# Performance work log

Measured on AMD Instinct MI355X. Metric: run time of the kernel, lower is better.

Reference implementation:

```python
import jax, jax.numpy as jnp
import numpy as np

EMBED_DIM = 1024
NUM_HEADS = 16
BLOCK_SIZE = 128
GLOBAL_EVERY = 24


def make_block_sparse_mask(seq_len):
    # 0 where allowed, -inf where disallowed. Allowed iff same block, or
    # either position lies in a 'global' block (block index % global_every == 0).
    bi = jnp.arange(seq_len) // BLOCK_SIZE
    is_global = (bi % GLOBAL_EVERY) == 0
    allowed = (bi[:, None] == bi[None, :]) | is_global[:, None] | is_global[None, :]
    return jnp.where(allowed, 0.0, -jnp.inf).astype(jnp.float32)


def setup_inputs() -> dict:
    key = jax.random.key(0)
    k_x, k_w, k_wo = jax.random.split(key, 3)
    B, L, D = 1, 4096, EMBED_DIM
    x = jax.random.normal(k_x, (B, L, D), dtype=jnp.float32)
    # nn.MultiheadAttention params: packed in_proj [3D, D] + bias [3D], out_proj [D, D] + bias [D]
    w_qkv = jax.random.normal(k_w, (3 * D, D), dtype=jnp.float32) * 0.02
    b_qkv = jnp.zeros((3 * D,), dtype=jnp.float32)
    w_out = jax.random.normal(k_wo, (D, D), dtype=jnp.float32) * 0.02
    b_out = jnp.zeros((D,), dtype=jnp.float32)
    return {"x": x, "w_qkv": w_qkv, "b_qkv": b_qkv, "w_out": w_out, "b_out": b_out}


def reference(x, w_qkv, b_qkv, w_out, b_out):
    B, L, D = x.shape
    H = NUM_HEADS
    hd = D // H
    mask = make_block_sparse_mask(L)  # [L, L] additive
    qkv = x @ w_qkv.T + b_qkv  # [B, L, 3D]
    q, k, v = jnp.split(qkv, 3, axis=-1)
    # [B, H, L, hd]
    q = q.reshape(B, L, H, hd).transpose(0, 2, 1, 3)
    k = k.reshape(B, L, H, hd).transpose(0, 2, 1, 3)
    v = v.reshape(B, L, H, hd).transpose(0, 2, 1, 3)
    scale = 1.0 / jnp.sqrt(jnp.asarray(hd, dtype=x.dtype))
    scores = jnp.einsum('bhqd,bhkd->bhqk', q * scale, k) + mask  # [B, H, L, L]
    attn = jax.nn.softmax(scores, axis=-1)
    out = jnp.einsum('bhqk,bhkd->bhqd', attn, v)  # [B, H, L, hd]
    out = out.transpose(0, 2, 1, 3).reshape(B, L, D)
    return out @ w_out.T + b_out
```

## Files before the change

### kernel.cpp

```cpp
#include <hip/hip_runtime.h>
#include <hip/hip_bf16.h>
#include <math.h>


#define SEQ 4096
#define DIM 1024
#define NHEADS 16
#define HDIM 64
#define BS 128
#define ESTRIDE 136

using short8 = __attribute__((ext_vector_type(8))) short;
using floatx4 = __attribute__((ext_vector_type(4))) float;

__device__ __forceinline__ float bf2f(short s) {
  unsigned u = ((unsigned)(unsigned short)s) << 16;
  return __uint_as_float(u);
}

__device__ __forceinline__ unsigned pack_bf16(float a, float b) {
  __hip_bfloat16 ba = __float2bfloat16(a);
  __hip_bfloat16 bb = __float2bfloat16(b);
  return ((unsigned)*(unsigned short*)&bb << 16) | (unsigned)*(unsigned short*)&ba;
}

__device__ __forceinline__ void gld_lds16(const __hip_bfloat16* g, __hip_bfloat16* l) {
  __builtin_amdgcn_global_load_lds(
      (const __attribute__((address_space(1))) unsigned int*)g,
      (__attribute__((address_space(3))) unsigned int*)l, 16, 0, 0);
}

__global__ __launch_bounds__(256) void downcast3(
    const float* __restrict__ x, const float* __restrict__ wq,
    const float* __restrict__ wo, __hip_bfloat16* __restrict__ xd,
    __hip_bfloat16* __restrict__ wqd, __hip_bfloat16* __restrict__ wod) {
  int id = blockIdx.x;
  const float* src;
  __hip_bfloat16* dst;
  int base;
  if (id < 4096) { src = x; dst = xd; base = id; }
  else if (id < 7168) { src = wq; dst = wqd; base = id - 4096; }
  else { src = wo; dst = wod; base = id - 7168; }
  int i = (base * 256 + threadIdx.x) * 4;
  float4 v = *(const float4*)(src + i);
  __hip_bfloat16 b0 = __float2bfloat16(v.x);
  __hip_bfloat16 b1 = __float2bfloat16(v.y);
  __hip_bfloat16 b2 = __float2bfloat16(v.z);
  __hip_bfloat16 b3 = __float2bfloat16(v.w);
  ushort4 packed = {*(unsigned short*)&b0, *(unsigned short*)&b1,
                    *(unsigned short*)&b2, *(unsigned short*)&b3};
  *(ushort4*)(((unsigned short*)dst) + i) = packed;
}

__global__ __launch_bounds__(256) void gemm_qkv(const __hip_bfloat16* __restrict__ Amat,
                                                const __hip_bfloat16* __restrict__ Wmat,
                                                const float* __restrict__ Bias,
                                                __hip_bfloat16* __restrict__ qkv) {
  __shared__ __align__(16) char pool[128 * ESTRIDE * 2];
  __hip_bfloat16* Asmem = (__hip_bfloat16*)pool;
  __hip_bfloat16* Bsmem = (__hip_bfloat16*)(pool + 8192);
  __hip_bfloat16* Ep = (__hip_bfloat16*)pool;

  const int Kd = DIM;
  const int t = threadIdx.x;
  const int w = t >> 6;
  const int lane = t & 63;
  const int fr = lane & 15;
  const int quad = lane >> 4;
  const int wm = w >> 1, wn = w & 1;

  int id = blockIdx.x;
  int xcd = id & 7, j = id >> 3;
  int m_idx = xcd + (j & 3) * 8;
  int n_idx = j >> 2;
  const int m0 = m_idx * 128;
  const int n0 = n_idx * 128;
  const int s = n0 >> 10;
  const int cc0 = n0 & 1023;
  const bool vmode = (s == 2);

  const __hip_bfloat16* APtr = vmode ? Amat + (size_t)m0 * Kd : Wmat + (size_t)n0 * Kd;
  const __hip_bfloat16* BPtr = vmode ? Wmat + (size_t)n0 * Kd : Amat + (size_t)m0 * Kd;

  floatx4 acc[4][4];
#pragma unroll
  for (int i = 0; i < 4; ++i)
#pragma unroll
    for (int jj = 0; jj < 4; ++jj) acc[i][jj] = (floatx4){0.f, 0.f, 0.f, 0.f};

  for (int kk = 0; kk < Kd / 32; ++kk) {
#pragma unroll
    for (int jj = 0; jj < 2; ++jj) {
      int c = jj * 256 + t;
      int ldso = (jj * 256 + w * 64) * 8;
      gld_lds16(APtr + (size_t)(c >> 2) * Kd + kk * 32 + (c & 3) * 8, &Asmem[ldso]);
      gld_lds16(BPtr + (size_t)(c >> 2) * Kd + kk * 32 + (c & 3) * 8, &Bsmem[ldso]);
    }
    __syncthreads();
    short8 af[4], bf_[4];
#pragma unroll
    for (int mt = 0; mt < 4; ++mt)
      af[mt] = *(const short8*)&Asmem[(wm * 64 + mt * 16 + fr) * 32 + quad * 8];
#pragma unroll
    for (int nt = 0; nt < 4; ++nt)
      bf_[nt] = *(const short8*)&Bsmem[(wn * 64 + nt * 16 + fr) * 32 + quad * 8];
#pragma unroll
    for (int mt = 0; mt < 4; ++mt)
#pragma unroll
      for (int nt = 0; nt < 4; ++nt)
        acc[mt][nt] = __builtin_amdgcn_mfma_f32_16x16x32_bf16(af[mt], bf_[nt],
                                                              acc[mt][nt], 0, 0, 0);
    __syncthreads();
  }

#pragma unroll
  for (int nt = 0; nt < 4; ++nt) {
    int dcol = wn * 64 + nt * 16 + fr;
#pragma unroll
    for (int mt = 0; mt < 4; ++mt) {
      int drow0 = wm * 64 + mt * 16 + quad * 4;
      ushort4 pk;
      unsigned short* pks = (unsigned short*)&pk;
#pragma unroll
      for (int i = 0; i < 4; ++i) {
        __hip_bfloat16 bb = __float2bfloat16(acc[mt][nt][i]);
        pks[i] = *(unsigned short*)&bb;
      }
      *(ushort4*)&Ep[dcol * ESTRIDE + drow0] = pk;
    }
  }
  __syncthreads();

  if (!vmode) {
    __hip_bfloat16* dst = qkv + (size_t)s * SEQ * DIM;
#pragma unroll
    for (int rr = 0; rr < 8; ++rr) {
      int m = rr * 16 + (t >> 4);
      int ch = (t & 15) * 8;
      short8 v8 = *(const short8*)&Ep[m * ESTRIDE + ch];
      float4 b0 = *(const float4*)&Bias[n0 + ch];
      float4 b1 = *(const float4*)&Bias[n0 + ch + 4];
      float bb[8] = {b0.x, b0.y, b0.z, b0.w, b1.x, b1.y, b1.z, b1.w};
      short8 o8;
#pragma unroll
      for (int k = 0; k < 8; ++k) {
        __hip_bfloat16 ob = __float2bfloat16(bf2f(v8[k]) + bb[k]);
        o8[k] = *(short*)&ob;
      }
      *(short8*)&dst[(size_t)(m0 + m) * DIM + cc0 + ch] = o8;
    }
  } else {
    __hip_bfloat16* vt = qkv + 2ull * SEQ * DIM;
#pragma unroll
    for (int rr = 0; rr < 8; ++rr) {
      int nrow = rr * 16 + (t >> 4);
      int ch = (t & 15) * 8;
      float bv = Bias[n0 + nrow];
      short8 v8 = *(const short8*)&Ep[nrow * ESTRIDE + ch];
      short8 o8;
#pragma unroll
      for (int k = 0; k < 8; ++k) {
        __hip_bfloat16 ob = __float2bfloat16(bf2f(v8[k]) + bv);
        o8[k] = *(short*)&ob;
      }
      *(short8*)&vt[(size_t)(cc0 + nrow) * SEQ + m0 + ch] = o8;
    }
  }
}

__global__ __launch_bounds__(256) void gemm_out(const __hip_bfloat16* __restrict__ Amat,
                                                const __hip_bfloat16* __restrict__ Wmat,
                                                const float* __restrict__ Bias,
                                                float* __restrict__ out) {
  __shared__ __align__(16) __hip_bfloat16 Asmem[128 * 32];
  __shared__ __align__(16) __hip_bfloat16 Bsmem[64 * 32];
  const int Kd = DIM;
  const int t = threadIdx.x;
  const int w = t >> 6;
  const int lane = t & 63;
  const int fr = lane & 15;
  const int quad = lane >> 4;
  const int wm = w >> 1, wn = w & 1;
  int id = blockIdx.x;
  int xcd = id & 7, j = id >> 3;
  int m_idx = xcd + (j & 3) * 8;
  int n_idx = j >> 2;
  const int m0 = m_idx * 128;
  const int n0 = n_idx * 64;
  const __hip_bfloat16* Ablk = Amat + (size_t)m0 * Kd;
  const __hip_bfloat16* Bblk = Wmat + (size_t)n0 * Kd;
  floatx4 acc[4][2];
#pragma unroll
  for (int i = 0; i < 4; ++i)
#pragma unroll
    for (int jj = 0; jj < 2; ++jj) acc[i][jj] = (floatx4){0.f, 0.f, 0.f, 0.f};
  for (int kk = 0; kk < Kd / 32; ++kk) {
#pragma unroll
    for (int jj = 0; jj < 2; ++jj) {
      int c = jj * 256 + t;
      int ldso = (jj * 256 + w * 64) * 8;
      gld_lds16(Ablk + (size_t)(c >> 2) * Kd + kk * 32 + (c & 3) * 8, &Asmem[ldso]);
    }
    gld_lds16(Bblk + (size_t)(t >> 2) * Kd + kk * 32 + (t & 3) * 8, &Bsmem[t * 8]);
    __syncthreads();
    short8 af[4], bf_[2];
#pragma unroll
    for (int mt = 0; mt < 4; ++mt)
      af[mt] = *(const short8*)&Asmem[(wm * 64 + mt * 16 + fr) * 32 + quad * 8];
#pragma unroll
    for (int nt = 0; nt < 2; ++nt)
      bf_[nt] = *(const short8*)&Bsmem[(wn * 32 + nt * 16 + fr) * 32 + quad * 8];
#pragma unroll
    for (int mt = 0; mt < 4; ++mt)
#pragma unroll
      for (int nt = 0; nt < 2; ++nt)
        acc[mt][nt] = __builtin_amdgcn_mfma_f32_16x16x32_bf16(af[mt], bf_[nt],
                                                              acc[mt][nt], 0, 0, 0);
    __syncthreads();
  }
#pragma unroll
  for (int nt = 0; nt < 2; ++nt) {
    int n = n0 + wn * 32 + nt * 16 + fr;
    float bv = Bias[n];
#pragma unroll
    for (int mt = 0; mt < 4; ++mt) {
      int m = m0 + wm * 64 + mt * 16 + quad * 4;
#pragma unroll
      for (int i = 0; i < 4; ++i)
        out[(size_t)(m + i) * DIM + n] = acc[mt][nt][i] + bv;
    }
  }
}

__global__ __launch_bounds__(256) void attn_mfma(
    const __hip_bfloat16* __restrict__ qkv,
    __hip_bfloat16* __restrict__ aout,
    float* __restrict__ po, float* __restrict__ pm, float* __restrict__ pl) {
  __shared__ __align__(16) __hip_bfloat16 Kbuf[16 * 512];
  __shared__ __align__(16) __hip_bfloat16 Vbuf[16 * 512];
  const int h = blockIdx.y;
  const int wgid = blockIdx.x;
  const int t = threadIdx.x;
  const int wv = t >> 6;
  const int lane = t & 63;
  const int fr = lane & 15;
  const int quad = lane >> 4;

  int qb, q0, niter, slice = 0, pid = 0;
  bool direct;
  if (wgid < 32) {
    int gi = wgid;
    slice = gi & 7;
    int chunk = gi >> 3;
    qb = (chunk >> 1) * 24;
    q0 = qb * BS + (chunk & 1) * 64;
    niter = 4;
    direct = false;
    pid = (h * 4 + chunk) * 8 + slice;
  } else {
    int nb = (wgid - 32) >> 1;
    qb = (nb < 23) ? nb + 1 : nb + 2;
    q0 = qb * BS + ((wgid - 32) & 1) * 64;
    niter = 3;
    direct = true;
  }

  const __hip_bfloat16* Q = qkv;
  const __hip_bfloat16* K = qkv + (size_t)SEQ * DIM;
  const __hip_bfloat16* Vt = qkv + 2ull * SEQ * DIM;

  short8 qa0, qa1;
  {
    const __hip_bfloat16* qp =
        Q + (size_t)(q0 + wv * 16 + fr) * DIM + h * HDIM + quad * 8;
    qa0 = *(const short8*)(qp);
    qa1 = *(const short8*)(qp + 32);
  }

  float mrow = -INFINITY, lsum = 0.f;
  floatx4 o[4];
#pragma unroll
  for (int i = 0; i < 4; ++i) o[i] = (floatx4){0.f, 0.f, 0.f, 0.f};

  for (int bi = 0; bi < niter; ++bi) {
    int kb = direct ? (bi == 0 ? 0 : (bi == 1 ? qb : 24)) : slice * 4 + bi;

    const __hip_bfloat16* Kg = K + (size_t)(kb * BS) * DIM + h * HDIM;
    const __hip_bfloat16* Vg = Vt + (size_t)(h * HDIM) * SEQ + kb * BS;
    __syncthreads();
#pragma unroll
    for (int rr = 0; rr < 4; ++rr) {
      int f = rr * 4 + wv;
      int nt = f >> 1, ks = f & 1;
      gld_lds16(Kg + (size_t)(nt * 16 + fr) * DIM + ks * 32 + quad * 8,
                &Kbuf[f * 512]);
      int nt2 = f >> 2, ks2 = f & 3;
      gld_lds16(Vg + (size_t)(nt2 * 16 + fr) * SEQ + ks2 * 32 + quad * 8,
                &Vbuf[f * 512]);
    }
    __syncthreads();

    floatx4 s[8];
#pragma unroll
    for (int nt = 0; nt < 8; ++nt) {
      short8 kf0 = *(const short8*)&Kbuf[(nt * 2 + 0) * 512 + lane * 8];
      short8 kf1 = *(const short8*)&Kbuf[(nt * 2 + 1) * 512 + lane * 8];
      floatx4 acc = {0.f, 0.f, 0.f, 0.f};
      acc = __builtin_amdgcn_mfma_f32_16x16x32_bf16(kf0, qa0, acc, 0, 0, 0);
      acc = __builtin_amdgcn_mfma_f32_16x16x32_bf16(kf1, qa1, acc, 0, 0, 0);
      s[nt] = acc;
    }

    float mr[8];
#pragma unroll
    for (int nt = 0; nt < 8; ++nt)
      mr[nt] = fmaxf(fmaxf(s[nt][0], s[nt][1]), fmaxf(s[nt][2], s[nt][3]));
    float m01 = fmaxf(mr[0], mr[1]), m23 = fmaxf(mr[2], mr[3]);
    float m45 = fmaxf(mr[4], mr[5]), m67 = fmaxf(mr[6], mr[7]);
    float rmax = fmaxf(fmaxf(m01, m23), fmaxf(m45, m67));
    rmax = fmaxf(rmax, __shfl_xor(rmax, 16, 64));
    rmax = fmaxf(rmax, __shfl_xor(rmax, 32, 64));
    float newm = fmaxf(mrow, rmax);
    float alpha = __expf((mrow - newm) * 0.125f);
    float nm = newm * 0.125f;
    float psum = 0.f;
    unsigned pki[8][2];
#pragma unroll
    for (int nt = 0; nt < 8; ++nt) {
      float p0 = __expf(fmaf(s[nt][0], 0.125f, -nm));
      float p1 = __expf(fmaf(s[nt][1], 0.125f, -nm));
      float p2 = __expf(fmaf(s[nt][2], 0.125f, -nm));
      float p3 = __expf(fmaf(s[nt][3], 0.125f, -nm));
      psum += (p0 + p1) + (p2 + p3);
      pki[nt][0] = pack_bf16(p0, p1);
      pki[nt][1] = pack_bf16(p2, p3);
    }
    psum += __shfl_xor(psum, 16, 64);
    psum += __shfl_xor(psum, 32, 64);
    lsum = lsum * alpha + psum;
    mrow = newm;
#pragma unroll
    for (int nt2 = 0; nt2 < 4; ++nt2)
#pragma unroll
      for (int i = 0; i < 4; ++i) o[nt2][i] *= alpha;

    union { int w4[4]; short8 s8; } pw[4];
#pragma unroll
    for (int ks2 = 0; ks2 < 4; ++ks2) {
#pragma unroll
      for (int p = 0; p < 4; ++p) {
        int srcl = fr + ((((quad & 1) << 1) + (p >> 1)) << 4);
        int lo = __shfl((int)pki[2 * ks2][p & 1], srcl, 64);
        int hi = __shfl((int)pki[2 * ks2 + 1][p & 1], srcl, 64);
        pw[ks2].w4[p] = (quad & 2) ? hi : lo;
      }
    }

#pragma unroll
    for (int nt2 = 0; nt2 < 4; ++nt2) {
#pragma unroll
      for (int ks2 = 0; ks2 < 4; ++ks2) {
        short8 vb = *(const short8*)&Vbuf[(nt2 * 4 + ks2) * 512 + lane * 8];
        o[nt2] = __builtin_amdgcn_mfma_f32_16x16x32_bf16(vb, pw[ks2].s8, o[nt2], 0, 0, 0);
      }
    }
  }

  if (direct) {
    float inv = 1.f / lsum;
    __hip_bfloat16* orow = aout + (size_t)(q0 + wv * 16 + fr) * DIM + h * HDIM + quad * 4;
#pragma unroll
    for (int nt2 = 0; nt2 < 4; ++nt2) {
      ushort4 pk;
      unsigned short* pks = (unsigned short*)&pk;
#pragma unroll
      for (int i = 0; i < 4; ++i) {
        __hip_bfloat16 ob = __float2bfloat16(o[nt2][i] * inv);
        pks[i] = *(unsigned short*)&ob;
      }
      *(ushort4*)(orow + nt2 * 16) = pk;
    }
  } else {
    float* pob = po + (size_t)pid * 4096 + (wv * 16 + fr) * 64 + quad * 4;
#pragma unroll
    for (int nt2 = 0; nt2 < 4; ++nt2) {
      float4 v = {o[nt2][0], o[nt2][1], o[nt2][2], o[nt2][3]};
      *(float4*)(pob + nt2 * 16) = v;
    }
    if (quad == 0) {
      pm[pid * 64 + wv * 16 + fr] = mrow * 0.125f;
      pl[pid * 64 + wv * 16 + fr] = lsum;
    }
  }
}

__global__ __launch_bounds__(256) void combine(const float* __restrict__ po,
                                               const float* __restrict__ pm,
                                               const float* __restrict__ pl,
                                               __hip_bfloat16* __restrict__ aout) {
  int b = blockIdx.x;
  int h = b >> 2, chunk = b & 3;
  int t = threadIdx.x;
  int row = t >> 2;
  int d0 = (t & 3) * 16;

  float m8[8];
  float newm = -INFINITY;
#pragma unroll
  for (int s = 0; s < 8; ++s) {
    m8[s] = pm[(b * 8 + s) * 64 + row];
    newm = fmaxf(newm, m8[s]);
  }
  float wgt[8], lsum = 0.f;
#pragma unroll
  for (int s = 0; s < 8; ++s) {
    wgt[s] = __expf(m8[s] - newm);
    lsum += pl[(b * 8 + s) * 64 + row] * wgt[s];
  }
  float acc[16];
#pragma unroll
  for (int jj = 0; jj < 16; ++jj) acc[jj] = 0.f;
#pragma unroll
  for (int s = 0; s < 8; ++s) {
    const float* src = po + ((size_t)(b * 8 + s) * 4096) + row * 64 + d0;
#pragma unroll
    for (int j4 = 0; j4 < 4; ++j4) {
      float4 v = *(const float4*)(src + j4 * 4);
      acc[j4 * 4 + 0] += wgt[s] * v.x;
      acc[j4 * 4 + 1] += wgt[s] * v.y;
      acc[j4 * 4 + 2] += wgt[s] * v.z;
      acc[j4 * 4 + 3] += wgt[s] * v.w;
    }
  }
  float inv = 1.f / lsum;
  int qrow = (chunk >> 1) * 3072 + (chunk & 1) * 64 + row;
#pragma unroll
  for (int jj = 0; jj < 16; ++jj)
    aout[(size_t)qrow * DIM + h * HDIM + d0 + jj] = __float2bfloat16(acc[jj] * inv);
}

extern "C" void kernel_launch(void* const* d_in, const int* in_sizes, int n_in,
                              void* d_out, int out_size, void* d_ws, size_t ws_size,
                              hipStream_t stream) {
  const float* x = (const float*)d_in[0];
  const float* w_qkv = (const float*)d_in[1];
  const float* b_qkv = (const float*)d_in[2];
  const float* w_out = (const float*)d_in[3];
  const float* b_out = (const float*)d_in[4];
  float* out = (float*)d_out;

  char* wsb = (char*)d_ws;
  __hip_bfloat16* qkv_ws = (__hip_bfloat16*)(wsb);
  __hip_bfloat16* x_bf = (__hip_bfloat16*)(wsb + 24ull * 1024 * 1024);
  __hip_bfloat16* wqkv_bf = (__hip_bfloat16*)(wsb + 32ull * 1024 * 1024);
  __hip_bfloat16* wout_bf = (__hip_bfloat16*)(wsb + 38ull * 1024 * 1024);
  __hip_bfloat16* attn_ws = (__hip_bfloat16*)(wsb + 40ull * 1024 * 1024);
  float* po = (float*)(wsb + 24ull * 1024 * 1024);
  float* pm = (float*)(wsb + 32ull * 1024 * 1024);
  float* pl = (float*)(wsb + 32ull * 1024 * 1024 + 131072);

  dim3 blk(256);
  downcast3<<<dim3(8192), blk, 0, stream>>>(x, w_qkv, w_out, x_bf, wqkv_bf, wout_bf);
  gemm_qkv<<<dim3(768), blk, 0, stream>>>(x_bf, wqkv_bf, b_qkv, qkv_ws);
  attn_mfma<<<dim3(92, NHEADS), blk, 0, stream>>>(qkv_ws, attn_ws, po, pm, pl);
  combine<<<dim3(64), blk, 0, stream>>>(po, pm, pl, attn_ws);
  gemm_out<<<dim3(512), blk, 0, stream>>>(attn_ws, wout_bf, b_out, out);
}
```

Baseline: 174.0 us.

## Process two 64-row query chunks per workgroup to reuse K/V tiles

Each attention workgroup now handles a full 128-row query block as two 64-row sub-chunks that share the same K/V tiles staged in LDS. This halves the grid and the global-to-LDS traffic for K and V, and amortises the barriers. The cost is twice the register state per thread (Q fragments, accumulators, softmax stats) and fewer workgroups, which may hurt occupancy and latency hiding.

```diff
diff --git a/kernel.cpp b/kernel.cpp
--- a/kernel.cpp
+++ b/kernel.cpp
@@ -246,41 +246,45 @@
   const int fr = lane & 15;
   const int quad = lane >> 4;
 
-  int qb, q0, niter, slice = 0, pid = 0;
+  int qb, niter, slice = 0, pid0 = 0;
   bool direct;
-  if (wgid < 32) {
+  if (wgid < 16) {
     int gi = wgid;
     slice = gi & 7;
-    int chunk = gi >> 3;
-    qb = (chunk >> 1) * 24;
-    q0 = qb * BS + (chunk & 1) * 64;
+    int pairid = gi >> 3;
+    qb = pairid * 24;
     niter = 4;
     direct = false;
-    pid = (h * 4 + chunk) * 8 + slice;
+    pid0 = (h * 4 + pairid * 2) * 8 + slice;
   } else {
-    int nb = (wgid - 32) >> 1;
+    int nb = wgid - 16;
     qb = (nb < 23) ? nb + 1 : nb + 2;
-    q0 = qb * BS + ((wgid - 32) & 1) * 64;
     niter = 3;
     direct = true;
   }
+  const int q0 = qb * BS;
 
   const __hip_bfloat16* Q = qkv;
   const __hip_bfloat16* K = qkv + (size_t)SEQ * DIM;
   const __hip_bfloat16* Vt = qkv + 2ull * SEQ * DIM;
 
-  short8 qa0, qa1;
+  short8 qa[2][2];
   {
     const __hip_bfloat16* qp =
         Q + (size_t)(q0 + wv * 16 + fr) * DIM + h * HDIM + quad * 8;
-    qa0 = *(const short8*)(qp);
-    qa1 = *(const short8*)(qp + 32);
-  }
-
-  float mrow = -INFINITY, lsum = 0.f;
-  floatx4 o[4];
-#pragma unroll
-  for (int i = 0; i < 4; ++i) o[i] = (floatx4){0.f, 0.f, 0.f, 0.f};
+    qa[0][0] = *(const short8*)(qp);
+    qa[0][1] = *(const short8*)(qp + 32);
+    qa[1][0] = *(const short8*)(qp + (size_t)64 * DIM);
+    qa[1][1] = *(const short8*)(qp + (size_t)64 * DIM + 32);
+  }
+
+  float mrow[2] = {-INFINITY, -INFINITY};
+  float lsum[2] = {0.f, 0.f};
+  floatx4 o[2][4];
+#pragma unroll
+  for (int cu = 0; cu < 2; ++cu)
+#pragma unroll
+    for (int i = 0; i < 4; ++i) o[cu][i] = (floatx4){0.f, 0.f, 0.f, 0.f};
 
   for (int bi = 0; bi < niter; ++bi) {
     int kb = direct ? (bi == 0 ? 0 : (bi == 1 ? qb : 24)) : slice * 4 + bi;
@@ -300,96 +304,108 @@
     }
     __syncthreads();
 
-    floatx4 s[8];
-#pragma unroll
-    for (int nt = 0; nt < 8; ++nt) {
-      short8 kf0 = *(const short8*)&Kbuf[(nt * 2 + 0) * 512 + lane * 8];
-      short8 kf1 = *(const short8*)&Kbuf[(nt * 2 + 1) * 512 + lane * 8];
-      floatx4 acc = {0.f, 0.f, 0.f, 0.f};
-      acc = __builtin_amdgcn_mfma_f32_16x16x32_bf16(kf0, qa0, acc, 0, 0, 0);
-      acc = __builtin_amdgcn_mfma_f32_16x16x32_bf16(kf1, qa1, acc, 0, 0, 0);
-      s[nt] = acc;
-    }
-
-    float mr[8];
-#pragma unroll
-    for (int nt = 0; nt < 8; ++nt)
-      mr[nt] = fmaxf(fmaxf(s[nt][0], s[nt][1]), fmaxf(s[nt][2], s[nt][3]));
-    float m01 = fmaxf(mr[0], mr[1]), m23 = fmaxf(mr[2], mr[3]);
-    float m45 = fmaxf(mr[4], mr[5]), m67 = fmaxf(mr[6], mr[7]);
-    float rmax = fmaxf(fmaxf(m01, m23), fmaxf(m45, m67));
-    rmax = fmaxf(rmax, __shfl_xor(rmax, 16, 64));
-    rmax = fmaxf(rmax, __shfl_xor(rmax, 32, 64));
-    float newm = fmaxf(mrow, rmax);
-    float alpha = __expf((mrow - newm) * 0.125f);
-    float nm = newm * 0.125f;
-    float psum = 0.f;
-    unsigned pki[8][2];
-#pragma unroll
-    for (int nt = 0; nt < 8; ++nt) {
-      float p0 = __expf(fmaf(s[nt][0], 0.125f, -nm));
-      float p1 = __expf(fmaf(s[nt][1], 0.125f, -nm));
-      float p2 = __expf(fmaf(s[nt][2], 0.125f, -nm));
-      float p3 = __expf(fmaf(s[nt][3], 0.125f, -nm));
-      psum += (p0 + p1) + (p2 + p3);
-      pki[nt][0] = pack_bf16(p0, p1);
-      pki[nt][1] = pack_bf16(p2, p3);
-    }
-    psum += __shfl_xor(psum, 16, 64);
-    psum += __shfl_xor(psum, 32, 64);
-    lsum = lsum * alpha + psum;
-    mrow = newm;
-#pragma unroll
-    for (int nt2 = 0; nt2 < 4; ++nt2)
-#pragma unroll
-      for (int i = 0; i < 4; ++i) o[nt2][i] *= alpha;
-
-    union { int w4[4]; short8 s8; } pw[4];
-#pragma unroll
-    for (int ks2 = 0; ks2 < 4; ++ks2) {
-#pragma unroll
-      for (int p = 0; p < 4; ++p) {
-        int srcl = fr + ((((quad & 1) << 1) + (p >> 1)) << 4);
-        int lo = __shfl((int)pki[2 * ks2][p & 1], srcl, 64);
-        int hi = __shfl((int)pki[2 * ks2 + 1][p & 1], srcl, 64);
-        pw[ks2].w4[p] = (quad & 2) ? hi : lo;
-      }
-    }
-
-#pragma unroll
-    for (int nt2 = 0; nt2 < 4; ++nt2) {
+#pragma unroll
+    for (int cu = 0; cu < 2; ++cu) {
+      floatx4 s[8];
+#pragma unroll
+      for (int nt = 0; nt < 8; ++nt) {
+        short8 kf0 = *(const short8*)&Kbuf[(nt * 2 + 0) * 512 + lane * 8];
+        short8 kf1 = *(const short8*)&Kbuf[(nt * 2 + 1) * 512 + lane * 8];
+        floatx4 acc = {0.f, 0.f, 0.f, 0.f};
+        acc = __builtin_amdgcn_mfma_f32_16x16x32_bf16(kf0, qa[cu][0], acc, 0, 0, 0);
+        acc = __builtin_amdgcn_mfma_f32_16x16x32_bf16(kf1, qa[cu][1], acc, 0, 0, 0);
+        s[nt] = acc;
+      }
+
+      float mr[8];
+#pragma unroll
+      for (int nt = 0; nt < 8; ++nt)
+        mr[nt] = fmaxf(fmaxf(s[nt][0], s[nt][1]), fmaxf(s[nt][2], s[nt][3]));
+      float m01 = fmaxf(mr[0], mr[1]), m23 = fmaxf(mr[2], mr[3]);
+      float m45 = fmaxf(mr[4], mr[5]), m67 = fmaxf(mr[6], mr[7]);
+      float rmax = fmaxf(fmaxf(m01, m23), fmaxf(m45, m67));
+      rmax = fmaxf(rmax, __shfl_xor(rmax, 16, 64));
+      rmax = fmaxf(rmax, __shfl_xor(rmax, 32, 64));
+      float newm = fmaxf(mrow[cu], rmax);
+      float alpha = __expf((mrow[cu] - newm) * 0.125f);
+      float nm = newm * 0.125f;
+      float psum = 0.f;
+      unsigned pki[8][2];
+#pragma unroll
+      for (int nt = 0; nt < 8; ++nt) {
+        float p0 = __expf(fmaf(s[nt][0], 0.125f, -nm));
+        float p1 = __expf(fmaf(s[nt][1], 0.125f, -nm));
+        float p2 = __expf(fmaf(s[nt][2], 0.125f, -nm));
+        float p3 = __expf(fmaf(s[nt][3], 0.125f, -nm));
+        psum += (p0 + p1) + (p2 + p3);
+        pki[nt][0] = pack_bf16(p0, p1);
+        pki[nt][1] = pack_bf16(p2, p3);
+      }
+      psum += __shfl_xor(psum, 16, 64);
+      psum += __shfl_xor(psum, 32, 64);
+      lsum[cu] = lsum[cu] * alpha + psum;
+      mrow[cu] = newm;
+#pragma unroll
+      for (int nt2 = 0; nt2 < 4; ++nt2)
+#pragma unroll
+        for (int i = 0; i < 4; ++i) o[cu][nt2][i] *= alpha;
+
+      union { int w4[4]; short8 s8; } pw[4];
 #pragma unroll
       for (int ks2 = 0; ks2 < 4; ++ks2) {
-        short8 vb = *(const short8*)&Vbuf[(nt2 * 4 + ks2) * 512 + lane * 8];
-        o[nt2] = __builtin_amdgcn_mfma_f32_16x16x32_bf16(vb, pw[ks2].s8, o[nt2], 0, 0, 0);
+#pragma unroll
+        for (int p = 0; p < 4; ++p) {
+          int srcl = fr + ((((quad & 1) << 1) + (p >> 1)) << 4);
+          int lo = __shfl((int)pki[2 * ks2][p & 1], srcl, 64);
+          int hi = __shfl((int)pki[2 * ks2 + 1][p & 1], srcl, 64);
+          pw[ks2].w4[p] = (quad & 2) ? hi : lo;
+        }
+      }
+
+#pragma unroll
+      for (int nt2 = 0; nt2 < 4; ++nt2) {
+#pragma unroll
+        for (int ks2 = 0; ks2 < 4; ++ks2) {
+          short8 vb = *(const short8*)&Vbuf[(nt2 * 4 + ks2) * 512 + lane * 8];
+          o[cu][nt2] = __builtin_amdgcn_mfma_f32_16x16x32_bf16(vb, pw[ks2].s8,
+                                                              o[cu][nt2], 0, 0, 0);
+        }
       }
     }
   }
 
   if (direct) {
-    float inv = 1.f / lsum;
-    __hip_bfloat16* orow = aout + (size_t)(q0 + wv * 16 + fr) * DIM + h * HDIM + quad * 4;
-#pragma unroll
-    for (int nt2 = 0; nt2 < 4; ++nt2) {
-      ushort4 pk;
-      unsigned short* pks = (unsigned short*)&pk;
-#pragma unroll
-      for (int i = 0; i < 4; ++i) {
-        __hip_bfloat16 ob = __float2bfloat16(o[nt2][i] * inv);
-        pks[i] = *(unsigned short*)&ob;
-      }
-      *(ushort4*)(orow + nt2 * 16) = pk;
+#pragma unroll
+    for (int cu = 0; cu < 2; ++cu) {
+      float inv = 1.f / lsum[cu];
+      __hip_bfloat16* orow = aout +
+          (size_t)(q0 + cu * 64 + wv * 16 + fr) * DIM + h * HDIM + quad * 4;
+#pragma unroll
+      for (int nt2 = 0; nt2 < 4; ++nt2) {
+        ushort4 pk;
+        unsigned short* pks = (unsigned short*)&pk;
+#pragma unroll
+        for (int i = 0; i < 4; ++i) {
+          __hip_bfloat16 ob = __float2bfloat16(o[cu][nt2][i] * inv);
+          pks[i] = *(unsigned short*)&ob;
+        }
+        *(ushort4*)(orow + nt2 * 16) = pk;
+      }
     }
   } else {
-    float* pob = po + (size_t)pid * 4096 + (wv * 16 + fr) * 64 + quad * 4;
-#pragma unroll
-    for (int nt2 = 0; nt2 < 4; ++nt2) {
-      float4 v = {o[nt2][0], o[nt2][1], o[nt2][2], o[nt2][3]};
-      *(float4*)(pob + nt2 * 16) = v;
-    }
-    if (quad == 0) {
-      pm[pid * 64 + wv * 16 + fr] = mrow * 0.125f;
-      pl[pid * 64 + wv * 16 + fr] = lsum;
+#pragma unroll
+    for (int cu = 0; cu < 2; ++cu) {
+      int pid = pid0 + cu * 8;
+      float* pob = po + (size_t)pid * 4096 + (wv * 16 + fr) * 64 + quad * 4;
+#pragma unroll
+      for (int nt2 = 0; nt2 < 4; ++nt2) {
+        float4 v = {o[cu][nt2][0], o[cu][nt2][1], o[cu][nt2][2], o[cu][nt2][3]};
+        *(float4*)(pob + nt2 * 16) = v;
+      }
+      if (quad == 0) {
+        pm[pid * 64 + wv * 16 + fr] = mrow[cu] * 0.125f;
+        pl[pid * 64 + wv * 16 + fr] = lsum[cu];
+      }
     }
   }
 }
@@ -462,7 +478,7 @@
   dim3 blk(256);
   downcast3<<<dim3(8192), blk, 0, stream>>>(x, w_qkv, w_out, x_bf, wqkv_bf, wout_bf);
   gemm_qkv<<<dim3(768), blk, 0, stream>>>(x_bf, wqkv_bf, b_qkv, qkv_ws);
-  attn_mfma<<<dim3(92, NHEADS), blk, 0, stream>>>(qkv_ws, attn_ws, po, pm, pl);
+  attn_mfma<<<dim3(46, NHEADS), blk, 0, stream>>>(qkv_ws, attn_ws, po, pm, pl);
   combine<<<dim3(64), blk, 0, stream>>>(po, pm, pl, attn_ws);
   gemm_out<<<dim3(512), blk, 0, stream>>>(attn_ws, wout_bf, b_out, out);
 }
```

After: 188.7 us. 1.08x slower.
